# Optimization experiments

Hardware: AMD Instinct MI355X
Metric: run time of the kernel (lower is better)

Reference implementation:

```python
import jax, jax.numpy as jnp
import numpy as np

WS = (5, 3, 1)          # per-level window sizes (CrossLayerPosEmbedding3D default)
STRIDES = (4, 2, 1)
PADS = (2, 1, 0)
HWS = (80, 40, 20)      # per-level map sizes -> 20x20 = 400 windows per level
B, C, NH = 8, 256, 4
HD = C // NH            # head_dim = 64
NTOK = (25, 9, 1)       # tokens per level, total 35
W0 = WS[0]
TABLE = (2 * W0 - 1) ** 2  # 81


def _rel_pos_index():
    # replicates CrossLayerPosEmbedding3D (spatial=True): float cross-scale coords
    coords = []
    for i, w in enumerate(WS):
        c = (np.arange(w) - w // 2).astype(np.float64)
        if i < len(WS) - 1:
            c = c * (W0 / w)
        gh, gw = np.meshgrid(c, c, indexing='ij')
        coords.append(np.stack([gh.reshape(-1), gw.reshape(-1)]))
    cf = np.concatenate(coords, axis=-1)                       # (2, 35)
    rel = (cf[:, :, None] - cf[:, None, :]).transpose(1, 2, 0).copy()
    rel[..., 0] += W0 - 1
    rel[..., 1] += W0 - 1
    rel[..., 0] *= 2 * W0 - 1
    return rel.sum(-1).astype(np.float32)                      # (35, 35) float index

REL_IDX = _rel_pos_index()
LEVEL_OF_TOKEN = np.repeat(np.arange(3), NTOK)                 # (35,)


def unfold(x, k, s, p):
    # torch.nn.functional.unfold -> (B, n_windows, k*k, C) (overlaped_window_partition)
    Bx, Cx, H, W = x.shape
    xp = jnp.pad(x, ((0, 0), (0, 0), (p, p), (p, p)))
    oh = (H + 2 * p - k) // s + 1
    ow = (W + 2 * p - k) // s + 1
    hi = (np.arange(oh) * s)[:, None] + np.arange(k)           # (oh, k)
    wi = (np.arange(ow) * s)[:, None] + np.arange(k)           # (ow, k)
    pt = xp[:, :, hi[:, None, :, None], wi[None, :, None, :]]  # (B, C, oh, ow, k, k)
    return pt.transpose(0, 2, 3, 4, 5, 1).reshape(Bx, oh * ow, k * k, Cx)


def fold(win, H, W, k, s, p):
    # torch.nn.functional.fold (sums overlaps) (overlaped_window_reverse)
    Bx, Wm, _, Cx = win.shape
    oh = (H + 2 * p - k) // s + 1
    ow = (W + 2 * p - k) // s + 1
    Hp, Wp = H + 2 * p, W + 2 * p
    hi = (np.arange(oh) * s)[:, None] + np.arange(k)
    wi = (np.arange(ow) * s)[:, None] + np.arange(k)
    lin = (hi[:, None, :, None] * Wp + wi[None, :, None, :]).reshape(-1)
    vals = win.transpose(0, 3, 1, 2).reshape(Bx, Cx, -1)       # matches (Wm, k*k) flatten order
    canvas = jnp.zeros((Bx, Cx, Hp * Wp), win.dtype).at[:, :, lin].add(vals)
    return canvas.reshape(Bx, Cx, Hp, Wp)[:, :, p:p + H, p:p + W]


def _l2n(x):
    # F.normalize(dim=-1), eps=1e-12
    return x / jnp.maximum(jnp.linalg.norm(x, axis=-1, keepdims=True), 1e-12)


def _forward(x0, x1, x2, w_qkv0, w_qkv1, w_qkv2, w_proj, b_proj, rpb_table, abs_bias):
    xs = (x0, x1, x2)
    wq = (w_qkv0, w_qkv1, w_qkv2)
    qs, ks, vs = [], [], []
    for l in range(3):  # small fixed layer loop (structurally distinct weights)
        t = unfold(xs[l], WS[l], STRIDES[l], PADS[l])          # (B, 400, ws^2, C)
        qkv = jnp.einsum('bwtc,cf->bwtf', t, wq[l])
        Bx, Wm, T, _ = qkv.shape
        qkv = qkv.reshape(Bx, Wm, T, 3, NH, HD).transpose(3, 0, 4, 1, 2, 5)  # (3,B,H,Wm,t,hd)
        qs.append(qkv[0]); ks.append(qkv[1]); vs.append(qkv[2])
    q = jnp.concatenate(qs, axis=-2)                           # (B, H, 400, 35, hd)
    k = jnp.concatenate(ks, axis=-2)
    v = jnp.concatenate(vs, axis=-2)

    # interpolated cross-layer relative position bias (floor/ceil lerp on the table)
    idx = jnp.asarray(REL_IDX.reshape(-1))
    fl = jnp.clip(jnp.floor(idx).astype(jnp.int32), 0, TABLE - 1)
    ce = jnp.clip(jnp.ceil(idx).astype(jnp.int32), 0, TABLE - 1)
    wce = (idx - fl.astype(jnp.float32))[:, None]
    pos = (1.0 - wce) * rpb_table[fl] + wce * rpb_table[ce]    # (1225, NH)
    pos = pos.reshape(sum(NTOK), sum(NTOK), NH).transpose(2, 0, 1)  # (NH, 35, 35)
    # per-level absolute bias added on query-row blocks (torch cat over dim=-2)
    pos = pos + abs_bias[LEVEL_OF_TOKEN].T[:, :, None]

    attn = jnp.einsum('bhwqd,bhwkd->bhwqk', _l2n(q), _l2n(k)) + pos[None, :, None]
    attn = jax.nn.softmax(attn, axis=-1)
    out = jnp.einsum('bhwqk,bhwkd->bhwqd', attn, v)            # (B, H, 400, 35, hd)
    Bx = out.shape[0]
    out = out.transpose(0, 2, 3, 1, 4).reshape(Bx, -1, sum(NTOK), NH * HD)  # (B,400,35,C)
    out = jnp.einsum('bwtc,cf->bwtf', out, w_proj) + b_proj
    outs = jnp.split(out, np.cumsum(NTOK)[:-1].tolist(), axis=2)
    return tuple(fold(o, HWS[l], HWS[l], WS[l], STRIDES[l], PADS[l])
                 for l, o in enumerate(outs))


def setup_inputs() -> dict:
    key = jax.random.key(0)
    ks = jax.random.split(key, 8)
    return {
        'x0': jax.random.normal(ks[0], (B, C, 80, 80), jnp.float32),
        'x1': jax.random.normal(ks[1], (B, C, 40, 40), jnp.float32),
        'x2': jax.random.normal(ks[2], (B, C, 20, 20), jnp.float32),
        'w_qkv0': jax.random.normal(ks[3], (C, 3 * C), jnp.float32) * 0.02,
        'w_qkv1': jax.random.normal(ks[4], (C, 3 * C), jnp.float32) * 0.02,
        'w_qkv2': jax.random.normal(ks[5], (C, 3 * C), jnp.float32) * 0.02,
        'w_proj': jax.random.normal(ks[6], (C, C), jnp.float32) * 0.02,
        'b_proj': jnp.zeros((C,), jnp.float32),
        'rpb_table': jax.random.normal(ks[7], (TABLE, NH), jnp.float32) * 0.02,
        'abs_bias': jnp.zeros((3, NH), jnp.float32),
    }


def reference(x0, x1, x2, w_qkv0, w_qkv1, w_qkv2, w_proj, b_proj, rpb_table, abs_bias):
    return _forward(x0, x1, x2, w_qkv0, w_qkv1, w_qkv2, w_proj, b_proj, rpb_table, abs_bias)
```

## Files before the change

### kernel.cpp

```cpp
#include <hip/hip_runtime.h>
#include <math.h>

namespace {

typedef _Float16 half8v __attribute__((ext_vector_type(8)));
typedef _Float16 half4v __attribute__((ext_vector_type(4)));
typedef float    floatx4 __attribute__((ext_vector_type(4)));

constexpr int B   = 8;
constexpr int C   = 256;
constexpr int NH  = 4;
constexpr int HD  = 64;
constexpr int NWIN = 400;
constexpr int NT  = 35;
constexpr int QKVN = 768;
constexpr int RPB = NWIN * NT;

constexpr size_t QKV_B  = (size_t)8400 * QKVN * 2;
constexpr size_t OATT_B = (size_t)RPB * C * 2;
constexpr size_t YT_B   = (size_t)RPB * C * 4;
constexpr size_t PB_B   = QKV_B + OATT_B + YT_B;
constexpr size_t POS_B  = 19712;

__device__ inline void token_coord(int j, double& cy, double& cx) {
  if (j < 25)      { int ty = j / 5,  tx = j % 5;  cy = (double)(ty - 2); cx = (double)(tx - 2); }
  else if (j < 34) { int t = j - 25; int ty = t / 3, tx = t % 3;
                     cy = (double)(ty - 1) * (5.0 / 3.0); cx = (double)(tx - 1) * (5.0 / 3.0); }
  else             { cy = 0.0; cx = 0.0; }
}

__global__ void pos_kernel(const float* __restrict__ rpb, const float* __restrict__ ab,
                           float* __restrict__ pos) {
  int p = blockIdx.x * blockDim.x + threadIdx.x;
  if (p >= NH * NT * NT) return;
  int j = p % NT, i = (p / NT) % NT, h = p / (NT * NT);
  double cyi, cxi, cyj, cxj;
  token_coord(i, cyi, cxi);
  token_coord(j, cyj, cxj);
  float fidx = (float)(((cyi - cyj) + 4.0) * 9.0 + ((cxi - cxj) + 4.0));
  int fl = min(max((int)floorf(fidx), 0), 80);
  int ce = min(max((int)ceilf(fidx), 0), 80);
  float w = fidx - (float)fl;
  float pv = (1.0f - w) * rpb[fl * NH + h] + w * rpb[ce * NH + h];
  int li = (i < 25) ? 0 : ((i < 34) ? 1 : 2);
  pos[p] = pv + ab[li * NH + h];
}

__global__ __launch_bounds__(256) void qkv_gemm(const float* __restrict__ X0,
                                                const float* __restrict__ X1,
                                                const float* __restrict__ X2,
                                                const float* __restrict__ W0,
                                                const float* __restrict__ W1,
                                                const float* __restrict__ W2,
                                                _Float16* __restrict__ Y0,
                                                _Float16* __restrict__ Y1,
                                                _Float16* __restrict__ Y2,
                                                int mb0, int mb01, int g) {
  __shared__ _Float16 As[128][40];
  __shared__ _Float16 Bs[128][40];

  int mblk = blockIdx.x;
  const float* X; const float* W; _Float16* Y; int HW;
  if (mblk < mb0)       { X = X0; W = W0; Y = Y0; HW = 6400; }
  else if (mblk < mb01) { X = X1; W = W1; Y = Y1; HW = 1600; mblk -= mb0; }
  else                  { X = X2; W = W2; Y = Y2; HW =  400; mblk -= mb01; }
  const int Mg = g * HW;

  const int tid  = threadIdx.x;
  const int m0   = mblk * 128;
  const int n0   = blockIdx.y * 128;
  const int w    = tid >> 6;
  const int lane = tid & 63;
  const int quad = lane >> 4;
  const int mn   = lane & 15;

  int rl[2], koA[2];
  const float* abase[2];
  const float* bbase[2];
#pragma unroll
  for (int u = 0; u < 2; ++u) {
    int c = w * 2 + u;
    int ko = c & 3; koA[u] = ko;
    rl[u] = (c >> 2) * 64 + lane;
    int gm = min(m0 + rl[u], Mg - 1);
    int bb = gm / HW, pix = gm - bb * HW;
    abase[u] = X + ((size_t)bb * C + ko * 8) * HW + pix;
    bbase[u] = W + (size_t)(ko * 8) * QKVN + n0 + rl[u];
  }

  float av[2][8], bv[2][8];
  auto LOAD = [&](int k0) {
#pragma unroll
    for (int u = 0; u < 2; ++u) {
      const float* xp = abase[u] + (size_t)k0 * HW;
      const float* wp = bbase[u] + (size_t)k0 * QKVN;
#pragma unroll
      for (int j = 0; j < 8; ++j) { av[u][j] = xp[(size_t)j * HW]; bv[u][j] = wp[(size_t)j * QKVN]; }
    }
  };

  LOAD(0);
  floatx4 acc[2][8] = {};
  for (int k0 = 0; k0 < C; k0 += 32) {
#pragma unroll
    for (int u = 0; u < 2; ++u) {
      half8v ha, hb;
#pragma unroll
      for (int j = 0; j < 8; ++j) { ha[j] = (_Float16)av[u][j]; hb[j] = (_Float16)bv[u][j]; }
      *(half8v*)&As[rl[u]][koA[u] * 8] = ha;
      *(half8v*)&Bs[rl[u]][koA[u] * 8] = hb;
    }
    __syncthreads();
    if (k0 + 32 < C) LOAD(k0 + 32);
    half8v a0 = *(const half8v*)&As[w * 32 + mn][quad * 8];
    half8v a1 = *(const half8v*)&As[w * 32 + 16 + mn][quad * 8];
#pragma unroll
    for (int ni = 0; ni < 8; ++ni) {
      half8v bf = *(const half8v*)&Bs[ni * 16 + mn][quad * 8];
      acc[0][ni] = __builtin_amdgcn_mfma_f32_16x16x32_f16(a0, bf, acc[0][ni], 0, 0, 0);
      acc[1][ni] = __builtin_amdgcn_mfma_f32_16x16x32_f16(a1, bf, acc[1][ni], 0, 0, 0);
    }
    __syncthreads();
  }

  const bool do_norm = (n0 < 512);
#pragma unroll
  for (int mi = 0; mi < 2; ++mi) {
#pragma unroll
    for (int r = 0; r < 4; ++r) {
      float s0 = 0.f, s1 = 0.f;
#pragma unroll
      for (int ni = 0; ni < 4; ++ni) { float vv = acc[mi][ni][r]; s0 += vv * vv; }
#pragma unroll
      for (int ni = 4; ni < 8; ++ni) { float vv = acc[mi][ni][r]; s1 += vv * vv; }
      s0 += __shfl_xor(s0, 1); s1 += __shfl_xor(s1, 1);
      s0 += __shfl_xor(s0, 2); s1 += __shfl_xor(s1, 2);
      s0 += __shfl_xor(s0, 4); s1 += __shfl_xor(s1, 4);
      s0 += __shfl_xor(s0, 8); s1 += __shfl_xor(s1, 8);
      float sc0 = do_norm ? (1.f / fmaxf(sqrtf(s0), 1e-12f)) : 1.f;
      float sc1 = do_norm ? (1.f / fmaxf(sqrtf(s1), 1e-12f)) : 1.f;
      int row = m0 + w * 32 + mi * 16 + quad * 4 + r;
      if (row < Mg) {
#pragma unroll
        for (int ni = 0; ni < 8; ++ni)
          Y[(size_t)row * QKVN + n0 + ni * 16 + mn] =
              (_Float16)(acc[mi][ni][r] * (ni < 4 ? sc0 : sc1));
      }
    }
  }
}

__device__ inline const _Float16* token_row_ptr(int j, int wy, int wx, int b,
                                                const _Float16* q0, const _Float16* q1,
                                                const _Float16* q2) {
  if (j >= NT) return nullptr;
  int k_, s_, p_, Hl, t; const _Float16* base;
  if (j < 25)      { k_ = 5; s_ = 4; p_ = 2; Hl = 80; t = j;      base = q0; }
  else if (j < 34) { k_ = 3; s_ = 2; p_ = 1; Hl = 40; t = j - 25; base = q1; }
  else             { k_ = 1; s_ = 1; p_ = 0; Hl = 20; t = 0;      base = q2; }
  int ty = t / k_, tx = t % k_;
  int y = wy * s_ + ty - p_;
  int x = wx * s_ + tx - p_;
  if ((unsigned)y >= (unsigned)Hl || (unsigned)x >= (unsigned)Hl) return nullptr;
  return base + ((size_t)b * Hl * Hl + (size_t)y * Hl + x) * QKVN;
}

__global__ __launch_bounds__(256, 4) void attn_kernel(const _Float16* __restrict__ qkv0,
                                                      const _Float16* __restrict__ qkv1,
                                                      const _Float16* __restrict__ qkv2,
                                                      const float* __restrict__ pos,
                                                      _Float16* __restrict__ O) {
  const int blk = blockIdx.x;
  const int w   = blk % NWIN;
  const int b   = blk / NWIN;
  const int wy = w / 20, wx = w % 20;
  const int tid  = threadIdx.x;
  const int h    = tid >> 6;
  const int lane = tid & 63;
  const int i16  = lane & 15;
  const int q4   = lane >> 4;

  __shared__ __align__(16) _Float16 vrows[48][260];

#pragma unroll
  for (int e0 = 0; e0 < 1536; e0 += 256) {
    int e = e0 + tid;
    int j = e >> 5, cc = e & 31;
    half8v val = (half8v)(_Float16)0.f;
    if (j < NT) {
      const _Float16* rp = token_row_ptr(j, wy, wx, b, qkv0, qkv1, qkv2);
      if (rp) val = *(const half8v*)(rp + 512 + cc * 8);
    }
    *(half8v*)&vrows[j][cc * 8] = val;
  }

  half8v qf[3][2], kf[3][2];
#pragma unroll
  for (int t = 0; t < 3; ++t) {
    const _Float16* rp = token_row_ptr(t * 16 + i16, wy, wx, b, qkv0, qkv1, qkv2);
#pragma unroll
    for (int kc = 0; kc < 2; ++kc) {
      if (rp) {
        qf[t][kc] = *(const half8v*)(rp + h * HD + kc * 32 + q4 * 8);
        kf[t][kc] = *(const half8v*)(rp + 256 + h * HD + kc * 32 + q4 * 8);
      } else {
        qf[t][kc] = (half8v)(_Float16)0.f;
        kf[t][kc] = (half8v)(_Float16)0.f;
      }
    }
  }

  floatx4 s[3][3] = {};
#pragma unroll
  for (int kc = 0; kc < 2; ++kc)
#pragma unroll
    for (int tj = 0; tj < 3; ++tj)
#pragma unroll
      for (int ti = 0; ti < 3; ++ti)
        s[tj][ti] = __builtin_amdgcn_mfma_f32_16x16x32_f16(kf[tj][kc], qf[ti][kc], s[tj][ti], 0, 0, 0);

#pragma unroll
  for (int tj = 0; tj < 3; ++tj)
#pragma unroll
    for (int ti = 0; ti < 3; ++ti)
#pragma unroll
      for (int r = 0; r < 4; ++r) {
        int j = tj * 16 + q4 * 4 + r;
        int i = ti * 16 + i16;
        if (j < NT) { if (i < NT) s[tj][ti][r] += pos[(h * NT + i) * NT + j]; }
        else s[tj][ti][r] = -INFINITY;
      }

  half4v pa[3][3];
#pragma unroll
  for (int ti = 0; ti < 3; ++ti) {
    float m = s[0][ti][0];
#pragma unroll
    for (int tj = 0; tj < 3; ++tj)
#pragma unroll
      for (int r = 0; r < 4; ++r) m = fmaxf(m, s[tj][ti][r]);
    m = fmaxf(m, __shfl_xor(m, 16));
    m = fmaxf(m, __shfl_xor(m, 32));
    float sum = 0.f;
#pragma unroll
    for (int tj = 0; tj < 3; ++tj)
#pragma unroll
      for (int r = 0; r < 4; ++r) { float e = expf(s[tj][ti][r] - m); s[tj][ti][r] = e; sum += e; }
    sum += __shfl_xor(sum, 16);
    sum += __shfl_xor(sum, 32);
    float inv = 1.f / sum;
#pragma unroll
    for (int tj = 0; tj < 3; ++tj)
#pragma unroll
      for (int r = 0; r < 4; ++r) pa[tj][ti][r] = (_Float16)(s[tj][ti][r] * inv);
  }

  __syncthreads();

  half4v vb[3][4];
#pragma unroll
  for (int tj = 0; tj < 3; ++tj)
#pragma unroll
    for (int n = 0; n < 4; ++n)
#pragma unroll
      for (int kk = 0; kk < 4; ++kk)
        vb[tj][n][kk] = vrows[tj * 16 + q4 * 4 + kk][h * HD + n * 16 + i16];

  const size_t obase = ((size_t)(b * NWIN + w) * NT) * C + h * HD;
#pragma unroll
  for (int ti = 0; ti < 3; ++ti) {
    floatx4 o[4] = {};
#pragma unroll
    for (int tj = 0; tj < 3; ++tj)
#pragma unroll
      for (int n = 0; n < 4; ++n)
        o[n] = __builtin_amdgcn_mfma_f32_16x16x16f16(pa[tj][ti], vb[tj][n], o[n], 0, 0, 0);
#pragma unroll
    for (int r = 0; r < 4; ++r) {
      int i = ti * 16 + q4 * 4 + r;
      if (i < NT) {
#pragma unroll
        for (int n = 0; n < 4; ++n)
          O[obase + (size_t)i * C + n * 16 + i16] = (_Float16)o[n][r];
      }
    }
  }
}

__global__ __launch_bounds__(256) void proj_gemm(const _Float16* __restrict__ A,
                                                 const float* __restrict__ W,
                                                 const float* __restrict__ bias,
                                                 float* __restrict__ Yt, int Mg) {
  __shared__ __align__(16) char smem[128 * 69 * 4];
  _Float16 (*As)[40] = (_Float16(*)[40])smem;
  _Float16 (*Bs)[40] = (_Float16(*)[40])(smem + 128 * 40 * 2);
  float    (*Cs)[69] = (float(*)[69])smem;

  const int tid  = threadIdx.x;
  const int m0   = blockIdx.x * 128;
  const int n0   = blockIdx.y * 64;
  const int w    = tid >> 6;
  const int lane = tid & 63;
  const int quad = lane >> 4;
  const int mn   = lane & 15;

  int aM[2], aK8[2], aRow[2];
#pragma unroll
  for (int u = 0; u < 2; ++u) {
    int e = u * 256 + tid;
    aM[u] = e >> 2; aK8[u] = e & 3;
    aRow[u] = min(m0 + aM[u], Mg - 1);
  }

  half8v apre[2]; float bpre[8];
  auto PLOAD = [&](int k0) {
#pragma unroll
    for (int u = 0; u < 2; ++u)
      apre[u] = *(const half8v*)&A[(size_t)aRow[u] * C + k0 + 8 * aK8[u]];
    const float* wp = W + (size_t)(k0 + w * 8) * C + n0 + lane;
#pragma unroll
    for (int j = 0; j < 8; ++j) bpre[j] = wp[(size_t)j * C];
  };

  PLOAD(0);
  floatx4 acc[2][4] = {};
  for (int k0 = 0; k0 < C; k0 += 32) {
#pragma unroll
    for (int u = 0; u < 2; ++u) *(half8v*)&As[aM[u]][8 * aK8[u]] = apre[u];
    {
      half8v hv;
#pragma unroll
      for (int j = 0; j < 8; ++j) hv[j] = (_Float16)bpre[j];
      *(half8v*)&Bs[lane][w * 8] = hv;
    }
    __syncthreads();
    if (k0 + 32 < C) PLOAD(k0 + 32);
    half8v a0 = *(const half8v*)&As[w * 32 + mn][quad * 8];
    half8v a1 = *(const half8v*)&As[w * 32 + 16 + mn][quad * 8];
#pragma unroll
    for (int ni = 0; ni < 4; ++ni) {
      half8v bf = *(const half8v*)&Bs[ni * 16 + mn][quad * 8];
      acc[0][ni] = __builtin_amdgcn_mfma_f32_16x16x32_f16(a0, bf, acc[0][ni], 0, 0, 0);
      acc[1][ni] = __builtin_amdgcn_mfma_f32_16x16x32_f16(a1, bf, acc[1][ni], 0, 0, 0);
    }
    __syncthreads();
  }

#pragma unroll
  for (int mi = 0; mi < 2; ++mi)
#pragma unroll
    for (int r = 0; r < 4; ++r)
#pragma unroll
      for (int ni = 0; ni < 4; ++ni)
        Cs[w * 32 + mi * 16 + quad * 4 + r][ni * 16 + mn] =
            acc[mi][ni][r] + bias[n0 + ni * 16 + mn];
  __syncthreads();
#pragma unroll
  for (int u = 0; u < 32; ++u) {
    int e = u * 256 + tid;
    int ml = e & 127, cl = e >> 7;
    int m = m0 + ml;
    if (m < Mg) {
      int bb = m / RPB;
      int r = m - bb * RPB;
      Yt[((size_t)bb * C + n0 + cl) * RPB + r] = Cs[ml][cl];
    }
  }
}

__global__ __launch_bounds__(256) void fold_kernel(const float* __restrict__ Yt,
                                                   float* __restrict__ out,
                                                   int k_, int s_, int p_, int H_,
                                                   int toff, int total) {
  int idx = blockIdx.x * 256 + threadIdx.x;
  if (idx >= total) return;
  int x = idx % H_;
  int y = (idx / H_) % H_;
  int c = (idx / (H_ * H_)) % C;
  int b = idx / (C * H_ * H_);
  int py = y + p_, px = x + p_;
  int ay = py - k_ + 1;
  int wy_lo = ay <= 0 ? 0 : (ay + s_ - 1) / s_;
  int wy_hi = min(19, py / s_);
  int ax = px - k_ + 1;
  int wx_lo = ax <= 0 ? 0 : (ax + s_ - 1) / s_;
  int wx_hi = min(19, px / s_);
  const float* base = Yt + ((size_t)b * C + c) * RPB;
  float acc = 0.f;
  for (int wy = wy_lo; wy <= wy_hi; ++wy) {
    int tyy = py - wy * s_;
    for (int wx = wx_lo; wx <= wx_hi; ++wx) {
      int txx = px - wx * s_;
      acc += base[(wy * 20 + wx) * NT + toff + tyy * k_ + txx];
    }
  }
  out[idx] = acc;
}

}

extern "C" void kernel_launch(void* const* d_in, const int* in_sizes, int n_in,
                              void* d_out, int out_size, void* d_ws, size_t ws_size,
                              hipStream_t stream) {
  const float* x0    = (const float*)d_in[0];
  const float* x1    = (const float*)d_in[1];
  const float* x2    = (const float*)d_in[2];
  const float* wq0   = (const float*)d_in[3];
  const float* wq1   = (const float*)d_in[4];
  const float* wq2   = (const float*)d_in[5];
  const float* wproj = (const float*)d_in[6];
  const float* bproj = (const float*)d_in[7];
  const float* rpb   = (const float*)d_in[8];
  const float* ab    = (const float*)d_in[9];
  float* out = (float*)d_out;

  int g = 8;
  while (g > 1 && POS_B + (size_t)g * PB_B > ws_size) g >>= 1;

  char* ws = (char*)d_ws;
  float*    posb  = (float*)ws;
  _Float16* qkv0g = (_Float16*)(ws + POS_B);
  _Float16* qkv1g = qkv0g + (size_t)g * 6400 * QKVN;
  _Float16* qkv2g = qkv1g + (size_t)g * 1600 * QKVN;
  _Float16* oatt  = qkv2g + (size_t)g *  400 * QKVN;
  float*    yt    = (float*)(ws + POS_B + (size_t)g * (QKV_B + OATT_B));

  pos_kernel<<<(NH * NT * NT + 255) / 256, 256, 0, stream>>>(rpb, ab, posb);

  const size_t off1 = (size_t)B * C * 6400;
  const size_t off2 = off1 + (size_t)B * C * 1600;

  const int mb0 = (g * 6400 + 127) / 128;
  const int mb1 = (g * 1600 + 127) / 128;
  const int mb2 = (g *  400 + 127) / 128;

  for (int b0 = 0; b0 < B; b0 += g) {
    const float* x0g = x0 + (size_t)b0 * C * 6400;
    const float* x1g = x1 + (size_t)b0 * C * 1600;
    const float* x2g = x2 + (size_t)b0 * C * 400;

    qkv_gemm<<<dim3(mb0 + mb1 + mb2, QKVN / 128), 256, 0, stream>>>(
        x0g, x1g, x2g, wq0, wq1, wq2, qkv0g, qkv1g, qkv2g, mb0, mb0 + mb1, g);

    attn_kernel<<<g * NWIN, 256, 0, stream>>>(qkv0g, qkv1g, qkv2g, posb, oatt);

    proj_gemm<<<dim3((g * RPB + 127) / 128, C / 64), 256, 0, stream>>>(oatt, wproj, bproj, yt, g * RPB);

    const int tot0 = g * C * 6400;
    const int tot1 = g * C * 1600;
    const int tot2 = g * C * 400;
    fold_kernel<<<(tot0 + 255) / 256, 256, 0, stream>>>(yt, out + (size_t)b0 * C * 6400,        5, 4, 2, 80, 0,  tot0);
    fold_kernel<<<(tot1 + 255) / 256, 256, 0, stream>>>(yt, out + off1 + (size_t)b0 * C * 1600, 3, 2, 1, 40, 25, tot1);
    fold_kernel<<<(tot2 + 255) / 256, 256, 0, stream>>>(yt, out + off2 + (size_t)b0 * C * 400,  1, 1, 0, 20, 34, tot2);
  }
}
```

Baseline: 456.6 us.

## Pre-transpose inputs and QKV weights to fp16 row-major before GEMM

```diff
diff --git a/kernel.cpp b/kernel.cpp
--- a/kernel.cpp
+++ b/kernel.cpp
@@ -20,6 +20,8 @@
 constexpr size_t OATT_B = (size_t)RPB * C * 2;
 constexpr size_t YT_B   = (size_t)RPB * C * 4;
 constexpr size_t PB_B   = QKV_B + OATT_B + YT_B;
+constexpr size_t XT_B   = (size_t)8400 * C * 2;
+constexpr size_t WT_B   = (size_t)3 * QKVN * C * 2;
 constexpr size_t POS_B  = 19712;
 
 __device__ inline void token_coord(int j, double& cy, double& cx) {
@@ -46,12 +48,56 @@
   pos[p] = pv + ab[li * NH + h];
 }
 
-__global__ __launch_bounds__(256) void qkv_gemm(const float* __restrict__ X0,
-                                                const float* __restrict__ X1,
-                                                const float* __restrict__ X2,
-                                                const float* __restrict__ W0,
-                                                const float* __restrict__ W1,
-                                                const float* __restrict__ W2,
+__global__ __launch_bounds__(256) void xpose_kernel(const float* __restrict__ x0,
+                                                    const float* __restrict__ x1,
+                                                    const float* __restrict__ x2,
+                                                    const float* __restrict__ w0,
+                                                    const float* __restrict__ w1,
+                                                    const float* __restrict__ w2,
+                                                    _Float16* __restrict__ xt0,
+                                                    _Float16* __restrict__ xt1,
+                                                    _Float16* __restrict__ xt2,
+                                                    _Float16* __restrict__ wt,
+                                                    int c0, int c1, int c2, int c3, int c4,
+                                                    int g) {
+  int bx = blockIdx.x;
+  const float* src; _Float16* dst; int HWi, Mg, m0;
+  if (bx < c0)      { src = x0; dst = xt0; HWi = 6400; Mg = g * 6400; m0 = bx * 64; }
+  else if (bx < c1) { src = x1; dst = xt1; HWi = 1600; Mg = g * 1600; m0 = (bx - c0) * 64; }
+  else if (bx < c2) { src = x2; dst = xt2; HWi = 400;  Mg = g * 400;  m0 = (bx - c1) * 64; }
+  else if (bx < c3) { src = w0; dst = wt;                HWi = 768; Mg = 768; m0 = (bx - c2) * 64; }
+  else if (bx < c4) { src = w1; dst = wt + 768 * 256;    HWi = 768; Mg = 768; m0 = (bx - c3) * 64; }
+  else              { src = w2; dst = wt + 2 * 768 * 256; HWi = 768; Mg = 768; m0 = (bx - c4) * 64; }
+
+  __shared__ _Float16 t[64][257];
+  const int tid = threadIdx.x;
+
+  const int p4 = (tid & 15) * 4;
+#pragma unroll
+  for (int it = 0; it < 16; ++it) {
+    int c = it * 16 + (tid >> 4);
+    int pg = m0 + p4;
+    int pgc = min(pg, Mg - 4);
+    int bb = pgc / HWi, pix = pgc - bb * HWi;
+    floatx4 v = *(const floatx4*)(src + ((size_t)bb * C + c) * HWi + pix);
+#pragma unroll
+    for (int i = 0; i < 4; ++i) t[p4 + i][c] = (_Float16)v[i];
+  }
+  __syncthreads();
+
+#pragma unroll
+  for (int e0 = 0; e0 < 8; ++e0) {
+    int e = e0 * 256 + tid;
+    int p = e >> 5, c8 = e & 31;
+    if (m0 + p < Mg)
+      *(half8v*)(dst + (size_t)(m0 + p) * C + c8 * 8) = *(const half8v*)&t[p][c8 * 8];
+  }
+}
+
+__global__ __launch_bounds__(256) void qkv_gemm(const _Float16* __restrict__ Xt0,
+                                                const _Float16* __restrict__ Xt1,
+                                                const _Float16* __restrict__ Xt2,
+                                                const _Float16* __restrict__ Wt,
                                                 _Float16* __restrict__ Y0,
                                                 _Float16* __restrict__ Y1,
                                                 _Float16* __restrict__ Y2,
@@ -60,11 +106,10 @@
   __shared__ _Float16 Bs[128][40];
 
   int mblk = blockIdx.x;
-  const float* X; const float* W; _Float16* Y; int HW;
-  if (mblk < mb0)       { X = X0; W = W0; Y = Y0; HW = 6400; }
-  else if (mblk < mb01) { X = X1; W = W1; Y = Y1; HW = 1600; mblk -= mb0; }
-  else                  { X = X2; W = W2; Y = Y2; HW =  400; mblk -= mb01; }
-  const int Mg = g * HW;
+  const _Float16* Xt; const _Float16* WtL; _Float16* Y; int Mg;
+  if (mblk < mb0)       { Xt = Xt0; WtL = Wt;                Y = Y0; Mg = g * 6400; }
+  else if (mblk < mb01) { Xt = Xt1; WtL = Wt + 768 * 256;    Y = Y1; Mg = g * 1600; mblk -= mb0; }
+  else                  { Xt = Xt2; WtL = Wt + 2 * 768 * 256; Y = Y2; Mg = g * 400;  mblk -= mb01; }
 
   const int tid  = threadIdx.x;
   const int m0   = mblk * 128;
@@ -74,44 +119,35 @@
   const int quad = lane >> 4;
   const int mn   = lane & 15;
 
-  int rl[2], koA[2];
-  const float* abase[2];
-  const float* bbase[2];
+  int rr[2], k8[2];
+  size_t aOff[2], bOff[2];
 #pragma unroll
   for (int u = 0; u < 2; ++u) {
-    int c = w * 2 + u;
-    int ko = c & 3; koA[u] = ko;
-    rl[u] = (c >> 2) * 64 + lane;
-    int gm = min(m0 + rl[u], Mg - 1);
-    int bb = gm / HW, pix = gm - bb * HW;
-    abase[u] = X + ((size_t)bb * C + ko * 8) * HW + pix;
-    bbase[u] = W + (size_t)(ko * 8) * QKVN + n0 + rl[u];
-  }
-
-  float av[2][8], bv[2][8];
-  auto LOAD = [&](int k0) {
+    int e = u * 256 + tid;
+    rr[u] = e >> 2; k8[u] = e & 3;
+    aOff[u] = (size_t)min(m0 + rr[u], Mg - 1) * C + k8[u] * 8;
+    bOff[u] = (size_t)(n0 + rr[u]) * C + k8[u] * 8;
+  }
+
+  half8v apre[2], bpre[2];
+  auto PLOAD = [&](int k0) {
 #pragma unroll
     for (int u = 0; u < 2; ++u) {
-      const float* xp = abase[u] + (size_t)k0 * HW;
-      const float* wp = bbase[u] + (size_t)k0 * QKVN;
-#pragma unroll
-      for (int j = 0; j < 8; ++j) { av[u][j] = xp[(size_t)j * HW]; bv[u][j] = wp[(size_t)j * QKVN]; }
+      apre[u] = *(const half8v*)(Xt + aOff[u] + k0);
+      bpre[u] = *(const half8v*)(WtL + bOff[u] + k0);
     }
   };
 
-  LOAD(0);
+  PLOAD(0);
   floatx4 acc[2][8] = {};
   for (int k0 = 0; k0 < C; k0 += 32) {
 #pragma unroll
     for (int u = 0; u < 2; ++u) {
-      half8v ha, hb;
-#pragma unroll
-      for (int j = 0; j < 8; ++j) { ha[j] = (_Float16)av[u][j]; hb[j] = (_Float16)bv[u][j]; }
-      *(half8v*)&As[rl[u]][koA[u] * 8] = ha;
-      *(half8v*)&Bs[rl[u]][koA[u] * 8] = hb;
+      *(half8v*)&As[rr[u]][k8[u] * 8] = apre[u];
+      *(half8v*)&Bs[rr[u]][k8[u] * 8] = bpre[u];
     }
     __syncthreads();
-    if (k0 + 32 < C) LOAD(k0 + 32);
+    if (k0 + 32 < C) PLOAD(k0 + 32);
     half8v a0 = *(const half8v*)&As[w * 32 + mn][quad * 8];
     half8v a1 = *(const half8v*)&As[w * 32 + 16 + mn][quad * 8];
 #pragma unroll
@@ -415,7 +451,7 @@
   float* out = (float*)d_out;
 
   int g = 8;
-  while (g > 1 && POS_B + (size_t)g * PB_B > ws_size) g >>= 1;
+  while (g > 1 && POS_B + (size_t)g * (PB_B + XT_B) + WT_B > ws_size) g >>= 1;
 
   char* ws = (char*)d_ws;
   float*    posb  = (float*)ws;
@@ -424,6 +460,10 @@
   _Float16* qkv2g = qkv1g + (size_t)g * 1600 * QKVN;
   _Float16* oatt  = qkv2g + (size_t)g *  400 * QKVN;
   float*    yt    = (float*)(ws + POS_B + (size_t)g * (QKV_B + OATT_B));
+  _Float16* xt0   = (_Float16*)(ws + POS_B + (size_t)g * PB_B);
+  _Float16* xt1   = xt0 + (size_t)g * 6400 * C;
+  _Float16* xt2   = xt1 + (size_t)g * 1600 * C;
+  _Float16* wt    = xt2 + (size_t)g *  400 * C;
 
   pos_kernel<<<(NH * NT * NT + 255) / 256, 256, 0, stream>>>(rpb, ab, posb);
 
@@ -433,14 +473,24 @@
   const int mb0 = (g * 6400 + 127) / 128;
   const int mb1 = (g * 1600 + 127) / 128;
   const int mb2 = (g *  400 + 127) / 128;
+
+  const int c0 = g * 100;
+  const int c1 = c0 + g * 25;
+  const int c2 = c1 + (g * 400 + 63) / 64;
+  const int c3 = c2 + 12;
+  const int c4 = c3 + 12;
+  const int c5 = c4 + 12;
 
   for (int b0 = 0; b0 < B; b0 += g) {
     const float* x0g = x0 + (size_t)b0 * C * 6400;
     const float* x1g = x1 + (size_t)b0 * C * 1600;
     const float* x2g = x2 + (size_t)b0 * C * 400;
 
+    xpose_kernel<<<c5, 256, 0, stream>>>(x0g, x1g, x2g, wq0, wq1, wq2,
+                                         xt0, xt1, xt2, wt, c0, c1, c2, c3, c4, g);
+
     qkv_gemm<<<dim3(mb0 + mb1 + mb2, QKVN / 128), 256, 0, stream>>>(
-        x0g, x1g, x2g, wq0, wq1, wq2, qkv0g, qkv1g, qkv2g, mb0, mb0 + mb1, g);
+        xt0, xt1, xt2, wt, qkv0g, qkv1g, qkv2g, mb0, mb0 + mb1, g);
 
     attn_kernel<<<g * NWIN, 256, 0, stream>>>(qkv0g, qkv1g, qkv2g, posb, oatt);
 
```

After: 464.9 us. Within noise of the previous version (+1.8%).

## Pre-transpose QKV weights to fp16 and keep full A tile resident across N tiles

Applied to the files above, without the earlier changes.

```diff
diff --git a/kernel.cpp b/kernel.cpp
--- a/kernel.cpp
+++ b/kernel.cpp
@@ -20,6 +20,7 @@
 constexpr size_t OATT_B = (size_t)RPB * C * 2;
 constexpr size_t YT_B   = (size_t)RPB * C * 4;
 constexpr size_t PB_B   = QKV_B + OATT_B + YT_B;
+constexpr size_t WT_B   = (size_t)3 * QKVN * C * 2;
 constexpr size_t POS_B  = 19712;
 
 __device__ inline void token_coord(int j, double& cy, double& cx) {
@@ -46,105 +47,133 @@
   pos[p] = pv + ab[li * NH + h];
 }
 
+__global__ __launch_bounds__(256) void wt_kernel(const float* __restrict__ w0,
+                                                 const float* __restrict__ w1,
+                                                 const float* __restrict__ w2,
+                                                 _Float16* __restrict__ wt) {
+  const int bx = blockIdx.x;
+  const float* src = bx < 12 ? w0 : (bx < 24 ? w1 : w2);
+  _Float16* dst = wt + (size_t)(bx / 12) * QKVN * C;
+  const int m0 = (bx % 12) * 64;
+  __shared__ _Float16 t[64][264];
+  const int tid = threadIdx.x;
+  const int p4 = (tid & 15) * 4;
+#pragma unroll
+  for (int it = 0; it < 16; ++it) {
+    int c = it * 16 + (tid >> 4);
+    floatx4 v = *(const floatx4*)(src + (size_t)c * QKVN + m0 + p4);
+#pragma unroll
+    for (int i = 0; i < 4; ++i) t[p4 + i][c] = (_Float16)v[i];
+  }
+  __syncthreads();
+#pragma unroll
+  for (int e0 = 0; e0 < 8; ++e0) {
+    int e = e0 * 256 + tid;
+    int p = e >> 5, c8 = e & 31;
+    *(half8v*)(dst + (size_t)(m0 + p) * C + c8 * 8) = *(const half8v*)&t[p][c8 * 8];
+  }
+}
+
 __global__ __launch_bounds__(256) void qkv_gemm(const float* __restrict__ X0,
                                                 const float* __restrict__ X1,
                                                 const float* __restrict__ X2,
-                                                const float* __restrict__ W0,
-                                                const float* __restrict__ W1,
-                                                const float* __restrict__ W2,
+                                                const _Float16* __restrict__ Wt,
                                                 _Float16* __restrict__ Y0,
                                                 _Float16* __restrict__ Y1,
                                                 _Float16* __restrict__ Y2,
                                                 int mb0, int mb01, int g) {
-  __shared__ _Float16 As[128][40];
+  __shared__ _Float16 As[128][264];
   __shared__ _Float16 Bs[128][40];
 
   int mblk = blockIdx.x;
-  const float* X; const float* W; _Float16* Y; int HW;
-  if (mblk < mb0)       { X = X0; W = W0; Y = Y0; HW = 6400; }
-  else if (mblk < mb01) { X = X1; W = W1; Y = Y1; HW = 1600; mblk -= mb0; }
-  else                  { X = X2; W = W2; Y = Y2; HW =  400; mblk -= mb01; }
+  const float* X; const _Float16* WtL; _Float16* Y; int HW;
+  if (mblk < mb0)       { X = X0; WtL = Wt;                 Y = Y0; HW = 6400; }
+  else if (mblk < mb01) { X = X1; WtL = Wt + QKVN * C;      Y = Y1; HW = 1600; mblk -= mb0; }
+  else                  { X = X2; WtL = Wt + 2 * QKVN * C;  Y = Y2; HW =  400; mblk -= mb01; }
   const int Mg = g * HW;
 
   const int tid  = threadIdx.x;
   const int m0   = mblk * 128;
-  const int n0   = blockIdx.y * 128;
   const int w    = tid >> 6;
   const int lane = tid & 63;
   const int quad = lane >> 4;
   const int mn   = lane & 15;
 
-  int rl[2], koA[2];
-  const float* abase[2];
-  const float* bbase[2];
-#pragma unroll
-  for (int u = 0; u < 2; ++u) {
-    int c = w * 2 + u;
-    int ko = c & 3; koA[u] = ko;
-    rl[u] = (c >> 2) * 64 + lane;
-    int gm = min(m0 + rl[u], Mg - 1);
+  {
+    const int r  = tid & 127;
+    const int ob = tid >> 7;
+    int gm = min(m0 + r, Mg - 1);
     int bb = gm / HW, pix = gm - bb * HW;
-    abase[u] = X + ((size_t)bb * C + ko * 8) * HW + pix;
-    bbase[u] = W + (size_t)(ko * 8) * QKVN + n0 + rl[u];
-  }
-
-  float av[2][8], bv[2][8];
-  auto LOAD = [&](int k0) {
-#pragma unroll
-    for (int u = 0; u < 2; ++u) {
-      const float* xp = abase[u] + (size_t)k0 * HW;
-      const float* wp = bbase[u] + (size_t)k0 * QKVN;
-#pragma unroll
-      for (int j = 0; j < 8; ++j) { av[u][j] = xp[(size_t)j * HW]; bv[u][j] = wp[(size_t)j * QKVN]; }
-    }
+    const float* xb = X + (size_t)bb * C * HW + pix;
+#pragma unroll
+    for (int i = 0; i < 16; ++i) {
+      int oct = ob + 2 * i;
+      const float* xp = xb + (size_t)oct * 8 * HW;
+      half8v hv;
+#pragma unroll
+      for (int j = 0; j < 8; ++j) hv[j] = (_Float16)xp[(size_t)j * HW];
+      *(half8v*)&As[r][oct * 8] = hv;
+    }
+  }
+
+  int rr[2], k8[2];
+#pragma unroll
+  for (int u = 0; u < 2; ++u) { int e = u * 256 + tid; rr[u] = e >> 2; k8[u] = e & 3; }
+
+  half8v bpre[2];
+  auto PLOAD = [&](int nt, int k0) {
+#pragma unroll
+    for (int u = 0; u < 2; ++u)
+      bpre[u] = *(const half8v*)(WtL + (size_t)(nt * 128 + rr[u]) * C + k8[u] * 8 + k0);
   };
 
-  LOAD(0);
-  floatx4 acc[2][8] = {};
-  for (int k0 = 0; k0 < C; k0 += 32) {
-#pragma unroll
-    for (int u = 0; u < 2; ++u) {
-      half8v ha, hb;
-#pragma unroll
-      for (int j = 0; j < 8; ++j) { ha[j] = (_Float16)av[u][j]; hb[j] = (_Float16)bv[u][j]; }
-      *(half8v*)&As[rl[u]][koA[u] * 8] = ha;
-      *(half8v*)&Bs[rl[u]][koA[u] * 8] = hb;
-    }
-    __syncthreads();
-    if (k0 + 32 < C) LOAD(k0 + 32);
-    half8v a0 = *(const half8v*)&As[w * 32 + mn][quad * 8];
-    half8v a1 = *(const half8v*)&As[w * 32 + 16 + mn][quad * 8];
-#pragma unroll
-    for (int ni = 0; ni < 8; ++ni) {
-      half8v bf = *(const half8v*)&Bs[ni * 16 + mn][quad * 8];
-      acc[0][ni] = __builtin_amdgcn_mfma_f32_16x16x32_f16(a0, bf, acc[0][ni], 0, 0, 0);
-      acc[1][ni] = __builtin_amdgcn_mfma_f32_16x16x32_f16(a1, bf, acc[1][ni], 0, 0, 0);
-    }
-    __syncthreads();
-  }
-
-  const bool do_norm = (n0 < 512);
-#pragma unroll
-  for (int mi = 0; mi < 2; ++mi) {
-#pragma unroll
-    for (int r = 0; r < 4; ++r) {
-      float s0 = 0.f, s1 = 0.f;
-#pragma unroll
-      for (int ni = 0; ni < 4; ++ni) { float vv = acc[mi][ni][r]; s0 += vv * vv; }
-#pragma unroll
-      for (int ni = 4; ni < 8; ++ni) { float vv = acc[mi][ni][r]; s1 += vv * vv; }
-      s0 += __shfl_xor(s0, 1); s1 += __shfl_xor(s1, 1);
-      s0 += __shfl_xor(s0, 2); s1 += __shfl_xor(s1, 2);
-      s0 += __shfl_xor(s0, 4); s1 += __shfl_xor(s1, 4);
-      s0 += __shfl_xor(s0, 8); s1 += __shfl_xor(s1, 8);
-      float sc0 = do_norm ? (1.f / fmaxf(sqrtf(s0), 1e-12f)) : 1.f;
-      float sc1 = do_norm ? (1.f / fmaxf(sqrtf(s1), 1e-12f)) : 1.f;
-      int row = m0 + w * 32 + mi * 16 + quad * 4 + r;
-      if (row < Mg) {
-#pragma unroll
-        for (int ni = 0; ni < 8; ++ni)
-          Y[(size_t)row * QKVN + n0 + ni * 16 + mn] =
-              (_Float16)(acc[mi][ni][r] * (ni < 4 ? sc0 : sc1));
+  PLOAD(0, 0);
+  __syncthreads();
+
+  for (int nt = 0; nt < 6; ++nt) {
+    floatx4 acc[2][8] = {};
+    for (int k0 = 0; k0 < C; k0 += 32) {
+#pragma unroll
+      for (int u = 0; u < 2; ++u) *(half8v*)&Bs[rr[u]][k8[u] * 8] = bpre[u];
+      __syncthreads();
+      int nk = k0 + 32, nn = nt;
+      if (nk == C) { nk = 0; nn = nt + 1; }
+      if (nn < 6) PLOAD(nn, nk);
+      half8v a0 = *(const half8v*)&As[w * 32 + mn][k0 + quad * 8];
+      half8v a1 = *(const half8v*)&As[w * 32 + 16 + mn][k0 + quad * 8];
+#pragma unroll
+      for (int ni = 0; ni < 8; ++ni) {
+        half8v bf = *(const half8v*)&Bs[ni * 16 + mn][quad * 8];
+        acc[0][ni] = __builtin_amdgcn_mfma_f32_16x16x32_f16(a0, bf, acc[0][ni], 0, 0, 0);
+        acc[1][ni] = __builtin_amdgcn_mfma_f32_16x16x32_f16(a1, bf, acc[1][ni], 0, 0, 0);
+      }
+      __syncthreads();
+    }
+
+    const int n0 = nt * 128;
+    const bool do_norm = (n0 < 512);
+#pragma unroll
+    for (int mi = 0; mi < 2; ++mi) {
+#pragma unroll
+      for (int r = 0; r < 4; ++r) {
+        float s0 = 0.f, s1 = 0.f;
+#pragma unroll
+        for (int ni = 0; ni < 4; ++ni) { float vv = acc[mi][ni][r]; s0 += vv * vv; }
+#pragma unroll
+        for (int ni = 4; ni < 8; ++ni) { float vv = acc[mi][ni][r]; s1 += vv * vv; }
+        s0 += __shfl_xor(s0, 1); s1 += __shfl_xor(s1, 1);
+        s0 += __shfl_xor(s0, 2); s1 += __shfl_xor(s1, 2);
+        s0 += __shfl_xor(s0, 4); s1 += __shfl_xor(s1, 4);
+        s0 += __shfl_xor(s0, 8); s1 += __shfl_xor(s1, 8);
+        float sc0 = do_norm ? (1.f / fmaxf(sqrtf(s0), 1e-12f)) : 1.f;
+        float sc1 = do_norm ? (1.f / fmaxf(sqrtf(s1), 1e-12f)) : 1.f;
+        int row = m0 + w * 32 + mi * 16 + quad * 4 + r;
+        if (row < Mg) {
+#pragma unroll
+          for (int ni = 0; ni < 8; ++ni)
+            Y[(size_t)row * QKVN + n0 + ni * 16 + mn] =
+                (_Float16)(acc[mi][ni][r] * (ni < 4 ? sc0 : sc1));
+        }
       }
     }
   }
@@ -415,7 +444,7 @@
   float* out = (float*)d_out;
 
   int g = 8;
-  while (g > 1 && POS_B + (size_t)g * PB_B > ws_size) g >>= 1;
+  while (g > 1 && POS_B + (size_t)g * PB_B + WT_B > ws_size) g >>= 1;
 
   char* ws = (char*)d_ws;
   float*    posb  = (float*)ws;
@@ -424,8 +453,10 @@
   _Float16* qkv2g = qkv1g + (size_t)g * 1600 * QKVN;
   _Float16* oatt  = qkv2g + (size_t)g *  400 * QKVN;
   float*    yt    = (float*)(ws + POS_B + (size_t)g * (QKV_B + OATT_B));
+  _Float16* wt    = (_Float16*)(ws + POS_B + (size_t)g * PB_B);
 
   pos_kernel<<<(NH * NT * NT + 255) / 256, 256, 0, stream>>>(rpb, ab, posb);
+  wt_kernel<<<36, 256, 0, stream>>>(wq0, wq1, wq2, wt);
 
   const size_t off1 = (size_t)B * C * 6400;
   const size_t off2 = off1 + (size_t)B * C * 1600;
@@ -439,8 +470,8 @@
     const float* x1g = x1 + (size_t)b0 * C * 1600;
     const float* x2g = x2 + (size_t)b0 * C * 400;
 
-    qkv_gemm<<<dim3(mb0 + mb1 + mb2, QKVN / 128), 256, 0, stream>>>(
-        x0g, x1g, x2g, wq0, wq1, wq2, qkv0g, qkv1g, qkv2g, mb0, mb0 + mb1, g);
+    qkv_gemm<<<mb0 + mb1 + mb2, 256, 0, stream>>>(
+        x0g, x1g, x2g, wt, qkv0g, qkv1g, qkv2g, mb0, mb0 + mb1, g);
 
     attn_kernel<<<g * NWIN, 256, 0, stream>>>(qkv0g, qkv1g, qkv2g, posb, oatt);
 
```

Result: slower. 474.4 us (+3.9%).
